# Kernel optimization log

Measured on AMD Instinct MI355X. Metric: run time of the kernel, lower is better.

## Reference

```python
import jax, jax.numpy as jnp
import numpy as np

EPS = 1e-08


def setup_inputs() -> dict:
    key = jax.random.key(0)
    k1, k2, k3 = jax.random.split(key, 3)
    n = 8192
    risk = jax.random.normal(k1, (n,), dtype=jnp.float32)
    t = jax.random.uniform(k2, (n,), dtype=jnp.float32)
    e = jax.random.randint(k3, (n,), 0, 2).astype(jnp.float32)
    return {"risk": risk, "t": t, "e": e}


def reference(risk, t, e):
    # R_mat[i, j] = (t[j] >= t[i])  -- risk set for sample i
    theta = risk.reshape(-1)                      # [n]
    exp_theta = jnp.exp(theta)                    # [n]
    R = (t[None, :] >= t[:, None]).astype(theta.dtype)  # [n, n]
    # sum over j of exp_theta[j] * R[i, j]
    log_sum = jnp.log(R @ exp_theta + EPS)        # [n]
    loss_cox = -jnp.mean((theta - log_sum) * e)
    return loss_cox
```

## Files before the change

kernel.cpp:

```cpp
#include <hip/hip_runtime.h>
#include <math.h>

#define N 8192
#define BS 256
#define NCHUNK 4
#define CHUNK (N / NCHUNK)
#define EPSV 1e-8f

__global__ __launch_bounds__(BS) void cox_partial(const float* __restrict__ risk,
                                                  const float* __restrict__ t,
                                                  float* __restrict__ Spart) {
    __shared__ float sT[CHUNK];
    __shared__ float sE[CHUNK];

    const int tid = threadIdx.x;
    const int chunk = blockIdx.y;

    const float4* t4g = (const float4*)t;
    const float4* r4g = (const float4*)risk;
    float4* sT4 = (float4*)sT;
    float4* sE4 = (float4*)sE;
    #pragma unroll
    for (int s = 0; s < CHUNK / 4 / BS; ++s) {
        int fl = tid + s * BS;
        int fg = chunk * (CHUNK / 4) + fl;
        float4 tv = t4g[fg];
        float4 rv = r4g[fg];
        sT4[fl] = tv;
        float4 ev;
        ev.x = __expf(rv.x);
        ev.y = __expf(rv.y);
        ev.z = __expf(rv.z);
        ev.w = __expf(rv.w);
        sE4[fl] = ev;
    }

    const int lane = tid & 63;
    const int wave = tid >> 6;
    const int i0 = blockIdx.x * 32 + wave * 8;

    float ti[8];
    #pragma unroll
    for (int m = 0; m < 8; ++m) ti[m] = t[i0 + m];

    float sum[8];
    #pragma unroll
    for (int m = 0; m < 8; ++m) sum[m] = 0.0f;

    __syncthreads();

    #pragma unroll
    for (int k = 0; k < CHUNK / 4 / 64; ++k) {
        int f = lane + (k << 6);
        float4 tj = sT4[f];
        float4 ej = sE4[f];
        #pragma unroll
        for (int m = 0; m < 8; ++m) {
            float s0 = (tj.x >= ti[m]) ? ej.x : 0.0f;
            float s1 = (tj.y >= ti[m]) ? ej.y : 0.0f;
            float s2 = (tj.z >= ti[m]) ? ej.z : 0.0f;
            float s3 = (tj.w >= ti[m]) ? ej.w : 0.0f;
            sum[m] += (s0 + s1) + (s2 + s3);
        }
    }

    float myS = 0.0f;
    #pragma unroll
    for (int m = 0; m < 8; ++m) {
        float v = sum[m];
        v += __shfl_xor(v, 32);
        v += __shfl_xor(v, 16);
        v += __shfl_xor(v, 8);
        v += __shfl_xor(v, 4);
        v += __shfl_xor(v, 2);
        v += __shfl_xor(v, 1);
        if (lane == m) myS = v;
    }

    if (lane < 8) {
        Spart[chunk * N + i0 + lane] = myS;
    }
}

__global__ __launch_bounds__(1024) void cox_final(const float* __restrict__ Spart,
                                                  const float* __restrict__ risk,
                                                  const float* __restrict__ e,
                                                  float* __restrict__ out) {
    const int tid = threadIdx.x;
    const int lane = tid & 63;
    const int wave = tid >> 6;

    float acc = 0.0f;
    #pragma unroll
    for (int r = 0; r < N / 1024; ++r) {
        int i = tid + r * 1024;
        float S = Spart[i] + Spart[N + i] + Spart[2 * N + i] + Spart[3 * N + i];
        acc += e[i] * (risk[i] - __logf(S + EPSV));
    }

    acc += __shfl_xor(acc, 32);
    acc += __shfl_xor(acc, 16);
    acc += __shfl_xor(acc, 8);
    acc += __shfl_xor(acc, 4);
    acc += __shfl_xor(acc, 2);
    acc += __shfl_xor(acc, 1);

    __shared__ float sW[16];
    if (lane == 0) sW[wave] = acc;
    __syncthreads();
    if (tid == 0) {
        float tot = 0.0f;
        #pragma unroll
        for (int x = 0; x < 16; ++x) tot += sW[x];
        out[0] = -tot * (1.0f / (float)N);
    }
}

extern "C" void kernel_launch(void* const* d_in, const int* in_sizes, int n_in,
                              void* d_out, int out_size, void* d_ws, size_t ws_size,
                              hipStream_t stream) {
    const float* risk = (const float*)d_in[0];
    const float* t    = (const float*)d_in[1];
    const float* e    = (const float*)d_in[2];
    float* out  = (float*)d_out;
    float* part = (float*)d_ws;

    dim3 grid(N / 32, NCHUNK);
    cox_partial<<<grid, BS, 0, stream>>>(risk, t, part);
    cox_final<<<1, 1024, 0, stream>>>(part, risk, e, out);
}
```

Measured before the change: 66.39 us.

## Fuse partial and final kernels via last-block atomic counter reduction

Merges the two kernel launches into one grid where each block writes its partial sums and then increments a two-level atomic counter (32 sub-counters plus a master). The block that arrives last does the final log-sum and mean reduction with vectorized float4 loads. This removes the second launch and the gap between kernels, at the cost of atomics and threadfences in every block plus a serial tail done by a single 256-thread block. The counters are never reset but rely on modulo-32 wraparound, so they stay consistent across repeated calls.

```diff
diff --git a/kernel.cpp b/kernel.cpp
--- a/kernel.cpp
+++ b/kernel.cpp
@@ -5,16 +5,25 @@
 #define BS 256
 #define NCHUNK 4
 #define CHUNK (N / NCHUNK)
+#define NBLK ((N / 32) * NCHUNK)
 #define EPSV 1e-8f
 
-__global__ __launch_bounds__(BS) void cox_partial(const float* __restrict__ risk,
+__device__ unsigned cox_sub_ctr[32];
+__device__ unsigned cox_master_ctr;
+
+__global__ __launch_bounds__(BS) void cox_onepass(const float* __restrict__ risk,
                                                   const float* __restrict__ t,
-                                                  float* __restrict__ Spart) {
+                                                  const float* __restrict__ e,
+                                                  float* __restrict__ Spart,
+                                                  float* __restrict__ out) {
     __shared__ float sT[CHUNK];
     __shared__ float sE[CHUNK];
+    __shared__ int sLast;
 
     const int tid = threadIdx.x;
-    const int chunk = blockIdx.y;
+    const int bid = blockIdx.x;
+    const int chunk = bid & (NCHUNK - 1);
+    const int iblk = bid >> 2;
 
     const float4* t4g = (const float4*)t;
     const float4* r4g = (const float4*)risk;
@@ -37,7 +46,7 @@
 
     const int lane = tid & 63;
     const int wave = tid >> 6;
-    const int i0 = blockIdx.x * 32 + wave * 8;
+    const int i0 = iblk * 32 + wave * 8;
 
     float ti[8];
     #pragma unroll
@@ -76,26 +85,47 @@
         v += __shfl_xor(v, 1);
         if (lane == m) myS = v;
     }
-
     if (lane < 8) {
         Spart[chunk * N + i0 + lane] = myS;
     }
-}
 
-__global__ __launch_bounds__(1024) void cox_final(const float* __restrict__ Spart,
-                                                  const float* __restrict__ risk,
-                                                  const float* __restrict__ e,
-                                                  float* __restrict__ out) {
-    const int tid = threadIdx.x;
-    const int lane = tid & 63;
-    const int wave = tid >> 6;
+    __syncthreads();
+    if (tid == 0) {
+        int last = 0;
+        __threadfence();
+        unsigned o = atomicAdd(&cox_sub_ctr[bid & 31], 1u);
+        if ((o & 31u) == 31u) {
+            __threadfence();
+            unsigned m = atomicAdd(&cox_master_ctr, 1u);
+            if ((m & 31u) == 31u) last = 1;
+        }
+        sLast = last;
+    }
+    __syncthreads();
+    if (!sLast) return;
+
+    __threadfence();
+
+    const float4* S0 = (const float4*)(Spart);
+    const float4* S1 = (const float4*)(Spart + N);
+    const float4* S2 = (const float4*)(Spart + 2 * N);
+    const float4* S3 = (const float4*)(Spart + 3 * N);
+    const float4* e4 = (const float4*)e;
 
     float acc = 0.0f;
     #pragma unroll
-    for (int r = 0; r < N / 1024; ++r) {
-        int i = tid + r * 1024;
-        float S = Spart[i] + Spart[N + i] + Spart[2 * N + i] + Spart[3 * N + i];
-        acc += e[i] * (risk[i] - __logf(S + EPSV));
+    for (int r = 0; r < N / 4 / BS; ++r) {
+        int f = tid + r * BS;
+        float4 a = S0[f], b = S1[f], c = S2[f], d = S3[f];
+        float4 rv = r4g[f], ev = e4[f];
+        float Sx = (a.x + b.x) + (c.x + d.x);
+        float Sy = (a.y + b.y) + (c.y + d.y);
+        float Sz = (a.z + b.z) + (c.z + d.z);
+        float Sw = (a.w + b.w) + (c.w + d.w);
+        acc += ev.x * (rv.x - __logf(Sx + EPSV));
+        acc += ev.y * (rv.y - __logf(Sy + EPSV));
+        acc += ev.z * (rv.z - __logf(Sz + EPSV));
+        acc += ev.w * (rv.w - __logf(Sw + EPSV));
     }
 
     acc += __shfl_xor(acc, 32);
@@ -105,14 +135,11 @@
     acc += __shfl_xor(acc, 2);
     acc += __shfl_xor(acc, 1);
 
-    __shared__ float sW[16];
+    __shared__ float sW[4];
     if (lane == 0) sW[wave] = acc;
     __syncthreads();
     if (tid == 0) {
-        float tot = 0.0f;
-        #pragma unroll
-        for (int x = 0; x < 16; ++x) tot += sW[x];
-        out[0] = -tot * (1.0f / (float)N);
+        out[0] = -((sW[0] + sW[1]) + (sW[2] + sW[3])) * (1.0f / (float)N);
     }
 }
 
@@ -125,7 +152,5 @@
     float* out  = (float*)d_out;
     float* part = (float*)d_ws;
 
-    dim3 grid(N / 32, NCHUNK);
-    cox_partial<<<grid, BS, 0, stream>>>(risk, t, part);
-    cox_final<<<1, 1024, 0, stream>>>(part, risk, e, out);
+    cox_onepass<<<dim3(NBLK), dim3(BS), 0, stream>>>(risk, t, e, part, out);
 }
```

Result: slower. 80.10 us (+20.7%).
